# Kernel tuning notes

Hardware: AMD Instinct MI355X
Metric: run time of the kernel (lower is better)

## Reference

```python
import jax, jax.numpy as jnp
import numpy as np

L, B, S, H = 24, 32, 512, 1024   # layers, batch, pad_size, bert hidden
D_IN, D1, D2 = L * H, 900, 40     # 24576 -> 900 -> 40 -> 1


def setup_inputs() -> dict:
    key = jax.random.key(0)
    ks = jax.random.split(key, 8)
    hidden_states = jax.random.normal(ks[0], (L, B, S, H), dtype=jnp.float32)
    # monotonically increasing subword start indices; 0 == "no word starts here"
    bert_token_starts = jnp.sort(
        jax.random.randint(ks[1], (B, S), 0, S, dtype=jnp.int64), axis=-1)
    W1 = jax.random.normal(ks[2], (D_IN, D1), dtype=jnp.float32) * 0.02
    b1 = jnp.zeros((D1,), dtype=jnp.float32)
    W2 = jax.random.normal(ks[3], (D1, D2), dtype=jnp.float32) * 0.02
    b2 = jnp.zeros((D2,), dtype=jnp.float32)
    W3 = jax.random.normal(ks[4], (D2, 1), dtype=jnp.float32) * 0.02
    b3 = jnp.zeros((1,), dtype=jnp.float32)
    return {
        "hidden_states": hidden_states,
        "W1": W1, "b1": b1, "W2": W2, "b2": b2, "W3": W3, "b3": b3,
        "bert_token_starts": bert_token_starts,
    }


def reference(hidden_states, W1, b1, W2, b2, W3, b3, bert_token_starts):
    # torch.cat over 24 layers along dim=2  ->  [B, S, 24*H] (layer-major feature order)
    x = jnp.moveaxis(hidden_states, 0, 2).reshape(
        hidden_states.shape[1], hidden_states.shape[2], -1)  # [B, S, 24576]
    h = jax.nn.relu(x @ W1 + b1)                # [B, S, 900]
    h = jax.nn.relu(h @ W2 + b2)                # [B, S, 40]
    pred_logits = jax.nn.sigmoid(h @ W3 + b3)[..., 0]  # squeeze(2) -> [B, S]
    # ragged gather: pred_labels[b][w] = pred_logits[b][starts[b][w]] where start != 0
    # (starts are always < pad_size here; the st/end while-loop in the original is dead code)
    valid = bert_token_starts != 0
    idx = jnp.clip(bert_token_starts, 0, pred_logits.shape[1] - 1)
    gathered = jnp.take_along_axis(pred_logits, idx, axis=1)
    pred_labels = jnp.where(valid, gathered, jnp.zeros((), dtype=pred_logits.dtype))
    return pred_labels
```

## Files before the change

### kernel.cpp

```cpp
#include <hip/hip_runtime.h>

typedef __attribute__((ext_vector_type(8))) short bf16x8;
typedef __attribute__((ext_vector_type(4))) float f32x4;

#define L_DIM 24
#define B_DIM 32
#define S_DIM 512
#define H_DIM 1024
#define M_DIM 16384
#define K_DIM 24576
#define N_REAL 900
#define NP 1024

__device__ __forceinline__ short f2bf(float f) {
  unsigned u = __builtin_bit_cast(unsigned, f);
  u += 0x7FFFu + ((u >> 16) & 1u);
  return (short)(u >> 16);
}

__global__ __launch_bounds__(512)
void compact1_kernel(const int* __restrict__ starts, int* __restrict__ upos,
                     int* __restrict__ counts) {
  __shared__ int sc[512];
  const int b = blockIdx.x, t = threadIdx.x;
  const int v = starts[b * 512 + t];
  const int prev = (t > 0) ? starts[b * 512 + t - 1] : -1;
  const int flag = (v != 0 && v != prev) ? 1 : 0;
  sc[t] = flag;
  __syncthreads();
#pragma unroll
  for (int off = 1; off < 512; off <<= 1) {
    const int x = (t >= off) ? sc[t - off] : 0;
    __syncthreads();
    sc[t] += x;
    __syncthreads();
  }
  upos[b * 512 + t] = flag ? (sc[t] - 1) : -1;
  if (t == 511) counts[b] = sc[511];
}

__global__ __launch_bounds__(256)
void compact2_kernel(const int* __restrict__ counts, int* __restrict__ offs,
                     int* __restrict__ meta, int* __restrict__ idx) {
  __shared__ int s0, s1;
  if (threadIdx.x == 0) {
    int acc = 0;
    for (int b = 0; b < 32; ++b) { offs[b] = acc; acc += counts[b]; }
    meta[0] = acc;
    meta[1] = (acc + 255) & ~255;
    s0 = acc; s1 = (acc + 255) & ~255;
  }
  __syncthreads();
  for (int j = s0 + threadIdx.x; j < s1; j += 256) idx[j] = 0;
}

__global__ __launch_bounds__(512)
void compact3_kernel(const int* __restrict__ starts, const int* __restrict__ upos,
                     const int* __restrict__ offs, int* __restrict__ idx) {
  const int b = blockIdx.x, t = threadIdx.x;
  const int p = upos[b * 512 + t];
  if (p >= 0) idx[offs[b] + p] = b * 512 + starts[b * 512 + t];
}

__global__ __launch_bounds__(256)
void conv_a_kernel(const float* __restrict__ hs, const int* __restrict__ idx,
                   const int* __restrict__ meta, unsigned short* __restrict__ a) {
  const int mcp = meta[1];
  for (int j = blockIdx.x; j < mcp; j += gridDim.x) {
    const int m = idx[j];
    const int b = m >> 9, s = m & 511;
    const int j7 = j & 7;
    unsigned short* dstRow = a + (size_t)j * K_DIM;
#pragma unroll
    for (int i = 0; i < 12; ++i) {
      const int g = threadIdx.x + i * 256;
      const int l = g >> 7;
      const int h = (g & 127) * 8;
      const float* src = hs + (((size_t)l * B_DIM + b) * S_DIM + s) * H_DIM + h;
      float4 f0 = *(const float4*)src;
      float4 f1 = *(const float4*)(src + 4);
      bf16x8 p;
      p[0] = f2bf(f0.x); p[1] = f2bf(f0.y); p[2] = f2bf(f0.z); p[3] = f2bf(f0.w);
      p[4] = f2bf(f1.x); p[5] = f2bf(f1.y); p[6] = f2bf(f1.z); p[7] = f2bf(f1.w);
      const int slot = (g & 7) ^ j7;
      *(bf16x8*)(dstRow + (g & ~7) * 8 + slot * 8) = p;
    }
  }
}

__global__ __launch_bounds__(256)
void prep_w1t_kernel(const float* __restrict__ w1, unsigned short* __restrict__ w1t) {
  __shared__ unsigned short t[64][72];
  const int n0 = blockIdx.x * 64;
  const int k0 = blockIdx.y * 64;
  const int tid = threadIdx.x;
  {
    const int nl = tid & 63;
    const int n = n0 + nl;
#pragma unroll
    for (int p = 0; p < 16; ++p) {
      const int kl = p * 4 + (tid >> 6);
      float v = (n < N_REAL) ? w1[(size_t)(k0 + kl) * N_REAL + n] : 0.f;
      t[nl][kl] = (unsigned short)f2bf(v);
    }
  }
  __syncthreads();
  {
    const int kl = tid & 63;
#pragma unroll
    for (int p = 0; p < 16; ++p) {
      const int nl2 = p * 4 + (tid >> 6);
      const int n = n0 + nl2;
      const int slot = ((kl >> 3) ^ (n & 7)) & 7;
      w1t[(size_t)n * K_DIM + k0 + slot * 8 + (kl & 7)] = t[nl2][kl];
    }
  }
}

__global__ __launch_bounds__(256)
void prep_small_kernel(const float* __restrict__ w2, const float* __restrict__ b1,
                       float* __restrict__ w2t, float* __restrict__ b1p) {
  const int i = blockIdx.x * 256 + threadIdx.x;
  if (i < 40 * NP) {
    const int j = i >> 10, k = i & (NP - 1);
    w2t[i] = (k < N_REAL) ? w2[(size_t)k * 40 + j] : 0.f;
  }
  const int t2 = i - 40 * NP;
  if (t2 >= 0 && t2 < NP)
    b1p[t2] = (t2 < N_REAL) ? b1[t2] : 0.f;
}

#define SBAR() do { __builtin_amdgcn_sched_barrier(0); __builtin_amdgcn_s_barrier(); __builtin_amdgcn_sched_barrier(0); } while (0)
#define WAIT_LGKM0() do { asm volatile("s_waitcnt lgkmcnt(0)" ::: "memory"); __builtin_amdgcn_sched_barrier(0); } while (0)
#define VMWAIT(N) do { asm volatile("s_waitcnt vmcnt(" #N ")" ::: "memory"); __builtin_amdgcn_sched_barrier(0); } while (0)

#define STAGE(DSTREG, GBASE, ROWBASE, HALF, TK) do {                                   \
  _Pragma("unroll")                                                                    \
  for (int _i = 0; _i < 2; ++_i) {                                                     \
    const int _ch = wid * 2 + _i;                                                      \
    const int _row = (HALF) * 128 + _ch * 8 + (lane >> 3);                             \
    __builtin_amdgcn_global_load_lds(                                                  \
      (const __attribute__((address_space(1))) void*)((GBASE) +                        \
          (size_t)((ROWBASE) + _row) * K_DIM + (TK) * 64 + (lane & 7) * 8),            \
      (__attribute__((address_space(3))) void*)((DSTREG) + (HALF) * 16384 + _ch * 1024), \
      16, 0, 0);                                                                       \
  }                                                                                    \
} while (0)

#define LDA4(AV, MIBASE, ABUF) do {                                                    \
  _Pragma("unroll")                                                                    \
  for (int _mi = 0; _mi < 4; ++_mi) {                                                  \
    _Pragma("unroll")                                                                  \
    for (int _kk = 0; _kk < 2; ++_kk) {                                                \
      const int _r = ((MIBASE) >> 2) * 128 + wr * 64 + _mi * 16 + r15;                 \
      AV[_mi][_kk] = *(const bf16x8*)((ABUF) + _r * 128 + (((_kk)*4 + hi4) ^ (_r & 7)) * 16); \
    }                                                                                  \
  }                                                                                    \
} while (0)

#define LDB2(BV, NIBASE, BBUF) do {                                                    \
  _Pragma("unroll")                                                                    \
  for (int _ni = 0; _ni < 2; ++_ni) {                                                  \
    _Pragma("unroll")                                                                  \
    for (int _kk = 0; _kk < 2; ++_kk) {                                                \
      const int _r = ((NIBASE) >> 1) * 128 + wc * 32 + _ni * 16 + r15;                 \
      BV[_ni][_kk] = *(const bf16x8*)((BBUF) + _r * 128 + (((_kk)*4 + hi4) ^ (_r & 7)) * 16); \
    }                                                                                  \
  }                                                                                    \
} while (0)

#define MFMA_Q(AV, BV, MIBASE, NIBASE) do {                                            \
  _Pragma("unroll")                                                                    \
  for (int _mi = 0; _mi < 4; ++_mi)                                                    \
    _Pragma("unroll")                                                                  \
    for (int _ni = 0; _ni < 2; ++_ni)                                                  \
      _Pragma("unroll")                                                                \
      for (int _kk = 0; _kk < 2; ++_kk)                                                \
        acc[(MIBASE) + _mi][(NIBASE) + _ni] = __builtin_amdgcn_mfma_f32_16x16x32_bf16( \
            AV[_mi][_kk], BV[_ni][_kk], acc[(MIBASE) + _mi][(NIBASE) + _ni], 0, 0, 0); \
} while (0)

#define TILE_BODY(T, AB, BB, ABN, BBN, S1, S2, S3, S4, W1STMT, W4STMT) do {            \
                                                                \
  LDA4(av, 0, (AB));                                                                   \
  LDB2(bv0, 0, (BB));                                                                  \
  if (S1) STAGE((ABN), a, m0, 1, (T) + 1);                                             \
  SBAR();                                                                              \
  WAIT_LGKM0();                                                                        \
  __builtin_amdgcn_s_setprio(1);                                                       \
  MFMA_Q(av, bv0, 0, 0);                                                               \
  __builtin_amdgcn_s_setprio(0);                                                       \
  W1STMT;                                                                              \
  SBAR();                                                                              \
                                                                \
  LDB2(bv1, 2, (BB));                                                                  \
  if (S2) STAGE((BBN), w1t, n0, 1, (T) + 1);                                           \
  SBAR();                                                                              \
  WAIT_LGKM0();                                                                        \
  __builtin_amdgcn_s_setprio(1);                                                       \
  MFMA_Q(av, bv1, 0, 2);                                                               \
  __builtin_amdgcn_s_setprio(0);                                                       \
  SBAR();                                                                              \
                                                                \
  LDA4(av, 4, (AB));                                                                   \
  if (S3) STAGE((BB), w1t, n0, 0, (T) + 2);                                            \
  SBAR();                                                                              \
  WAIT_LGKM0();                                                                        \
  __builtin_amdgcn_s_setprio(1);                                                       \
  MFMA_Q(av, bv1, 4, 2);                                                               \
  __builtin_amdgcn_s_setprio(0);                                                       \
  SBAR();                                                                              \
                                                                \
  if (S4) STAGE((AB), a, m0, 0, (T) + 2);                                              \
  SBAR();                                                                              \
  WAIT_LGKM0();                                                                        \
  __builtin_amdgcn_s_setprio(1);                                                       \
  MFMA_Q(av, bv0, 4, 0);                                                               \
  __builtin_amdgcn_s_setprio(0);                                                       \
  W4STMT;                                                                              \
  SBAR();                                                                              \
} while (0)

__global__ __launch_bounds__(512, 2)
void gemm1_8ph_kernel(const unsigned short* __restrict__ a,
                      const unsigned short* __restrict__ w1t,
                      const float* __restrict__ b1p,
                      const int* __restrict__ meta,
                      float* __restrict__ h1) {
  const int mcp = meta[1];

  const int hw = blockIdx.x;
  const int c = hw & 7;
  const int r = hw >> 3;
  const int mb = (r >> 2) * 8 + c;
  const int nb = r & 3;
  const int m0 = mb * 256;
  if (m0 >= mcp) return;
  const int n0 = nb * 256;

  extern __shared__ char L[];
  char* const Ab0 = L;
  char* const Bb0 = L + 32768;
  char* const Ab1 = L + 65536;
  char* const Bb1 = L + 65536 + 32768;

  const int tid = threadIdx.x;
  const int lane = tid & 63;
  const int wid = tid >> 6;
  const int wr = wid >> 2;
  const int wc = wid & 3;
  const int r15 = lane & 15;
  const int hi4 = lane >> 4;

  f32x4 acc[8][4] = {};
  bf16x8 av[4][2], bv0[2][2], bv1[2][2];

  STAGE(Bb0, w1t, n0, 0, 0);
  STAGE(Ab0, a, m0, 0, 0);
  STAGE(Ab0, a, m0, 1, 0);
  STAGE(Bb0, w1t, n0, 1, 0);
  STAGE(Bb1, w1t, n0, 0, 1);
  STAGE(Ab1, a, m0, 0, 1);
  VMWAIT(8);
  SBAR();

  for (int kt = 0; kt < 191; ++kt) {
    const int t = 2 * kt;
    TILE_BODY(t,     Ab0, Bb0, Ab1, Bb1, 1, 1, 1, 1, VMWAIT(6), VMWAIT(8));
    TILE_BODY(t + 1, Ab1, Bb1, Ab0, Bb0, 1, 1, 1, 1, VMWAIT(6), VMWAIT(8));
  }
  TILE_BODY(382, Ab0, Bb0, Ab1, Bb1, 1, 1, 0, 0, VMWAIT(6), VMWAIT(0));
  TILE_BODY(383, Ab1, Bb1, Ab0, Bb0, 0, 0, 0, 0, (void)0, (void)0);

#pragma unroll
  for (int mi = 0; mi < 8; ++mi) {
#pragma unroll
    for (int ni = 0; ni < 4; ++ni) {
      const int n = n0 + (ni >> 1) * 128 + wc * 32 + (ni & 1) * 16 + r15;
      const float bias = b1p[n];
#pragma unroll
      for (int rr = 0; rr < 4; ++rr) {
        const int m = m0 + (mi >> 2) * 128 + wr * 64 + (mi & 3) * 16 + hi4 * 4 + rr;
        const float v = acc[mi][ni][rr] + bias;
        h1[(size_t)m * NP + n] = v > 0.f ? v : 0.f;
      }
    }
  }
}

__global__ __launch_bounds__(256)
void layer23_kernel(const float* __restrict__ h1, const float* __restrict__ w2t,
                    const float* __restrict__ b2, const float* __restrict__ w3,
                    const float* __restrict__ b3, const int* __restrict__ idx,
                    const int* __restrict__ meta, float* __restrict__ logits) {
  const int j = (blockIdx.x * 256 + threadIdx.x) >> 6;
  if (j >= meta[0]) return;
  const int lane = threadIdx.x & 63;
  const float* hrow = h1 + (size_t)j * NP;
  float acc = 0.f;
  if (lane < 40) {
    const float* wrow = w2t + lane * NP;
    for (int k = 0; k < NP; k += 8) {
      float4 h0 = *(const float4*)(hrow + k);
      float4 h4 = *(const float4*)(hrow + k + 4);
      float4 w0 = *(const float4*)(wrow + k);
      float4 w4 = *(const float4*)(wrow + k + 4);
      acc += h0.x * w0.x + h0.y * w0.y + h0.z * w0.z + h0.w * w0.w;
      acc += h4.x * w4.x + h4.y * w4.y + h4.z * w4.z + h4.w * w4.w;
    }
    acc += b2[lane];
    acc = acc > 0.f ? acc : 0.f;
    acc *= w3[lane];
  }
#pragma unroll
  for (int off = 32; off > 0; off >>= 1)
    acc += __shfl_down(acc, off);
  if (lane == 0)
    logits[idx[j]] = 1.f / (1.f + expf(-(acc + b3[0])));
}

__global__ __launch_bounds__(256)
void gather_kernel(const int* __restrict__ starts, const float* __restrict__ logits,
                   float* __restrict__ out) {
  const int i = blockIdx.x * 256 + threadIdx.x;
  if (i >= M_DIM) return;
  const int st = starts[i];
  int idx = st;
  if (idx < 0) idx = 0;
  if (idx > S_DIM - 1) idx = S_DIM - 1;
  out[i] = (st != 0) ? logits[((i >> 9) << 9) + idx] : 0.f;
}

extern "C" void kernel_launch(void* const* d_in, const int* in_sizes, int n_in,
                              void* d_out, int out_size, void* d_ws, size_t ws_size,
                              hipStream_t stream) {
  const float* hs = (const float*)d_in[0];
  const float* W1 = (const float*)d_in[1];
  const float* b1 = (const float*)d_in[2];
  const float* W2 = (const float*)d_in[3];
  const float* b2 = (const float*)d_in[4];
  const float* W3 = (const float*)d_in[5];
  const float* b3 = (const float*)d_in[6];
  const int* starts = (const int*)d_in[7];
  float* out = (float*)d_out;
  char* ws = (char*)d_ws;

  const size_t A_BYTES   = (size_t)M_DIM * K_DIM * 2;
  const size_t W1T_BYTES = (size_t)NP * K_DIM * 2;
  const size_t H1_BYTES  = (size_t)M_DIM * NP * 4;
  const size_t W2T_BYTES = 40 * NP * 4;
  const size_t B1P_BYTES = NP * 4;
  const size_t LG_BYTES  = M_DIM * 4;

  unsigned short* a    = (unsigned short*)ws;
  unsigned short* w1t  = (unsigned short*)(ws + A_BYTES);
  char* h1c            = ws + A_BYTES + W1T_BYTES;
  float* h1            = (float*)h1c;
  float* w2t           = (float*)(ws + A_BYTES + W1T_BYTES + H1_BYTES);
  float* b1p           = (float*)(ws + A_BYTES + W1T_BYTES + H1_BYTES + W2T_BYTES);
  float* logits        = (float*)(ws + A_BYTES + W1T_BYTES + H1_BYTES + W2T_BYTES + B1P_BYTES);
  int* idx             = (int*)(ws + A_BYTES + W1T_BYTES + H1_BYTES + W2T_BYTES + B1P_BYTES + LG_BYTES);
  int* meta            = (int*)(ws + A_BYTES + W1T_BYTES + H1_BYTES + W2T_BYTES + B1P_BYTES + LG_BYTES + 65536);
  int* upos            = (int*)h1c;
  int* counts          = (int*)(h1c + 65536);
  int* offs            = (int*)(h1c + 65536 + 128);

  hipFuncSetAttribute((const void*)gemm1_8ph_kernel,
                      hipFuncAttributeMaxDynamicSharedMemorySize, 131072);

  compact1_kernel<<<32, 512, 0, stream>>>(starts, upos, counts);
  compact2_kernel<<<1, 256, 0, stream>>>(counts, offs, meta, idx);
  compact3_kernel<<<32, 512, 0, stream>>>(starts, upos, offs, idx);
  conv_a_kernel<<<2048, 256, 0, stream>>>(hs, idx, meta, a);
  prep_w1t_kernel<<<dim3(16, 384), 256, 0, stream>>>(W1, w1t);
  prep_small_kernel<<<164, 256, 0, stream>>>(W2, b1, w2t, b1p);
  gemm1_8ph_kernel<<<256, 512, 131072, stream>>>(a, w1t, b1p, meta, h1);
  layer23_kernel<<<4096, 256, 0, stream>>>(h1, w2t, b2, W3, b3, idx, meta, logits);
  gather_kernel<<<64, 256, 0, stream>>>(starts, logits, out);
}
```

Before: 1.218 ms.

## Split GEMM1 K dimension three ways and reduce partials in layer23

GEMM1 now splits the K loop into three chunks of 128 tiles, launching three times as many workgroups, each writing an unbiased fp32 partial panel into its own buffer. The layer23 kernel sums the three partials, adds the bias and applies ReLU before the second layer. The aim is to fill more CUs when the compacted M is small, since 256 workgroups left many CUs idle. The cost is triple the h1 write and read traffic and a larger workspace.

```diff
diff --git a/kernel.cpp b/kernel.cpp
--- a/kernel.cpp
+++ b/kernel.cpp
@@ -224,19 +224,20 @@
 __global__ __launch_bounds__(512, 2)
 void gemm1_8ph_kernel(const unsigned short* __restrict__ a,
                       const unsigned short* __restrict__ w1t,
-                      const float* __restrict__ b1p,
                       const int* __restrict__ meta,
-                      float* __restrict__ h1) {
+                      float* __restrict__ h1p) {
   const int mcp = meta[1];
+  const int n_panels = mcp >> 8;
 
   const int hw = blockIdx.x;
-  const int c = hw & 7;
-  const int r = hw >> 3;
-  const int mb = (r >> 2) * 8 + c;
-  const int nb = r & 3;
+  const int mb = hw / 12;
+  if (mb >= n_panels) return;
+  const int rem = hw - mb * 12;
+  const int nb = rem & 3;
+  const int kh = rem >> 2;
   const int m0 = mb * 256;
-  if (m0 >= mcp) return;
   const int n0 = nb * 256;
+  const int t0 = kh * 128;
 
   extern __shared__ char L[];
   char* const Ab0 = L;
@@ -255,58 +256,64 @@
   f32x4 acc[8][4] = {};
   bf16x8 av[4][2], bv0[2][2], bv1[2][2];
 
-  STAGE(Bb0, w1t, n0, 0, 0);
-  STAGE(Ab0, a, m0, 0, 0);
-  STAGE(Ab0, a, m0, 1, 0);
-  STAGE(Bb0, w1t, n0, 1, 0);
-  STAGE(Bb1, w1t, n0, 0, 1);
-  STAGE(Ab1, a, m0, 0, 1);
+  STAGE(Bb0, w1t, n0, 0, t0);
+  STAGE(Ab0, a, m0, 0, t0);
+  STAGE(Ab0, a, m0, 1, t0);
+  STAGE(Bb0, w1t, n0, 1, t0);
+  STAGE(Bb1, w1t, n0, 0, t0 + 1);
+  STAGE(Ab1, a, m0, 0, t0 + 1);
   VMWAIT(8);
   SBAR();
 
-  for (int kt = 0; kt < 191; ++kt) {
-    const int t = 2 * kt;
+  for (int kt = 0; kt < 63; ++kt) {
+    const int t = t0 + 2 * kt;
     TILE_BODY(t,     Ab0, Bb0, Ab1, Bb1, 1, 1, 1, 1, VMWAIT(6), VMWAIT(8));
     TILE_BODY(t + 1, Ab1, Bb1, Ab0, Bb0, 1, 1, 1, 1, VMWAIT(6), VMWAIT(8));
   }
-  TILE_BODY(382, Ab0, Bb0, Ab1, Bb1, 1, 1, 0, 0, VMWAIT(6), VMWAIT(0));
-  TILE_BODY(383, Ab1, Bb1, Ab0, Bb0, 0, 0, 0, 0, (void)0, (void)0);
-
+  TILE_BODY(t0 + 126, Ab0, Bb0, Ab1, Bb1, 1, 1, 0, 0, VMWAIT(6), VMWAIT(0));
+  TILE_BODY(t0 + 127, Ab1, Bb1, Ab0, Bb0, 0, 0, 0, 0, (void)0, (void)0);
+
+  float* dst = h1p + (size_t)kh * ((size_t)M_DIM * NP);
 #pragma unroll
   for (int mi = 0; mi < 8; ++mi) {
 #pragma unroll
     for (int ni = 0; ni < 4; ++ni) {
       const int n = n0 + (ni >> 1) * 128 + wc * 32 + (ni & 1) * 16 + r15;
-      const float bias = b1p[n];
 #pragma unroll
       for (int rr = 0; rr < 4; ++rr) {
         const int m = m0 + (mi >> 2) * 128 + wr * 64 + (mi & 3) * 16 + hi4 * 4 + rr;
-        const float v = acc[mi][ni][rr] + bias;
-        h1[(size_t)m * NP + n] = v > 0.f ? v : 0.f;
+        dst[(size_t)m * NP + n] = acc[mi][ni][rr];
       }
     }
   }
 }
 
 __global__ __launch_bounds__(256)
-void layer23_kernel(const float* __restrict__ h1, const float* __restrict__ w2t,
-                    const float* __restrict__ b2, const float* __restrict__ w3,
-                    const float* __restrict__ b3, const int* __restrict__ idx,
-                    const int* __restrict__ meta, float* __restrict__ logits) {
+void layer23_kernel(const float* __restrict__ h1p, const float* __restrict__ w2t,
+                    const float* __restrict__ b1p, const float* __restrict__ b2,
+                    const float* __restrict__ w3, const float* __restrict__ b3,
+                    const int* __restrict__ idx, const int* __restrict__ meta,
+                    float* __restrict__ logits) {
   const int j = (blockIdx.x * 256 + threadIdx.x) >> 6;
   if (j >= meta[0]) return;
   const int lane = threadIdx.x & 63;
-  const float* hrow = h1 + (size_t)j * NP;
+  const float* p0 = h1p + (size_t)j * NP;
+  const float* p1 = p0 + (size_t)M_DIM * NP;
+  const float* p2 = p1 + (size_t)M_DIM * NP;
   float acc = 0.f;
   if (lane < 40) {
     const float* wrow = w2t + lane * NP;
-    for (int k = 0; k < NP; k += 8) {
-      float4 h0 = *(const float4*)(hrow + k);
-      float4 h4 = *(const float4*)(hrow + k + 4);
+    for (int k = 0; k < NP; k += 4) {
+      float4 a0 = *(const float4*)(p0 + k);
+      float4 a1 = *(const float4*)(p1 + k);
+      float4 a2 = *(const float4*)(p2 + k);
+      float4 bb = *(const float4*)(b1p + k);
       float4 w0 = *(const float4*)(wrow + k);
-      float4 w4 = *(const float4*)(wrow + k + 4);
-      acc += h0.x * w0.x + h0.y * w0.y + h0.z * w0.z + h0.w * w0.w;
-      acc += h4.x * w4.x + h4.y * w4.y + h4.z * w4.z + h4.w * w4.w;
+      float x0 = a0.x + a1.x + a2.x + bb.x; x0 = x0 > 0.f ? x0 : 0.f;
+      float x1 = a0.y + a1.y + a2.y + bb.y; x1 = x1 > 0.f ? x1 : 0.f;
+      float x2 = a0.z + a1.z + a2.z + bb.z; x2 = x2 > 0.f ? x2 : 0.f;
+      float x3 = a0.w + a1.w + a2.w + bb.w; x3 = x3 > 0.f ? x3 : 0.f;
+      acc += x0 * w0.x + x1 * w0.y + x2 * w0.z + x3 * w0.w;
     }
     acc += b2[lane];
     acc = acc > 0.f ? acc : 0.f;
@@ -347,7 +354,7 @@
 
   const size_t A_BYTES   = (size_t)M_DIM * K_DIM * 2;
   const size_t W1T_BYTES = (size_t)NP * K_DIM * 2;
-  const size_t H1_BYTES  = (size_t)M_DIM * NP * 4;
+  const size_t H1P_BYTES = 3ull * M_DIM * NP * 4;
   const size_t W2T_BYTES = 40 * NP * 4;
   const size_t B1P_BYTES = NP * 4;
   const size_t LG_BYTES  = M_DIM * 4;
@@ -355,12 +362,12 @@
   unsigned short* a    = (unsigned short*)ws;
   unsigned short* w1t  = (unsigned short*)(ws + A_BYTES);
   char* h1c            = ws + A_BYTES + W1T_BYTES;
-  float* h1            = (float*)h1c;
-  float* w2t           = (float*)(ws + A_BYTES + W1T_BYTES + H1_BYTES);
-  float* b1p           = (float*)(ws + A_BYTES + W1T_BYTES + H1_BYTES + W2T_BYTES);
-  float* logits        = (float*)(ws + A_BYTES + W1T_BYTES + H1_BYTES + W2T_BYTES + B1P_BYTES);
-  int* idx             = (int*)(ws + A_BYTES + W1T_BYTES + H1_BYTES + W2T_BYTES + B1P_BYTES + LG_BYTES);
-  int* meta            = (int*)(ws + A_BYTES + W1T_BYTES + H1_BYTES + W2T_BYTES + B1P_BYTES + LG_BYTES + 65536);
+  float* h1p           = (float*)h1c;
+  float* w2t           = (float*)(ws + A_BYTES + W1T_BYTES + H1P_BYTES);
+  float* b1p           = (float*)(ws + A_BYTES + W1T_BYTES + H1P_BYTES + W2T_BYTES);
+  float* logits        = (float*)(ws + A_BYTES + W1T_BYTES + H1P_BYTES + W2T_BYTES + B1P_BYTES);
+  int* idx             = (int*)(ws + A_BYTES + W1T_BYTES + H1P_BYTES + W2T_BYTES + B1P_BYTES + LG_BYTES);
+  int* meta            = (int*)(ws + A_BYTES + W1T_BYTES + H1P_BYTES + W2T_BYTES + B1P_BYTES + LG_BYTES + 65536);
   int* upos            = (int*)h1c;
   int* counts          = (int*)(h1c + 65536);
   int* offs            = (int*)(h1c + 65536 + 128);
@@ -374,7 +381,7 @@
   conv_a_kernel<<<2048, 256, 0, stream>>>(hs, idx, meta, a);
   prep_w1t_kernel<<<dim3(16, 384), 256, 0, stream>>>(W1, w1t);
   prep_small_kernel<<<164, 256, 0, stream>>>(W2, b1, w2t, b1p);
-  gemm1_8ph_kernel<<<256, 512, 131072, stream>>>(a, w1t, b1p, meta, h1);
-  layer23_kernel<<<4096, 256, 0, stream>>>(h1, w2t, b2, W3, b3, idx, meta, logits);
+  gemm1_8ph_kernel<<<768, 512, 131072, stream>>>(a, w1t, meta, h1p);
+  layer23_kernel<<<4096, 256, 0, stream>>>(h1p, w2t, b1p, b2, W3, b3, idx, meta, logits);
   gather_kernel<<<64, 256, 0, stream>>>(starts, logits, out);
 }
```

Result: no change. 1.241 ms (+1.9%).

## Shrink GEMM1 M-tile to 192 rows to cut padding waste and balance CUs

Applied to the files above, without the earlier changes.

Changes the first-layer GEMM tile from 256x256 to 192x256. The compacted row count is now padded to a multiple of 192 instead of 256, and the grid grows to 352 blocks. The A staging, LDS layout, MFMA quadrant schedule and pipeline wait counts are reworked to match, and the workspace is enlarged to cover the extra padded rows. The aim is less wasted compute on padded rows and a better spread of blocks over the CUs. The cost is lower per-block arithmetic intensity, more B reloads and a retuned pipeline that may stall differently.

```diff
diff --git a/kernel.cpp b/kernel.cpp
--- a/kernel.cpp
+++ b/kernel.cpp
@@ -11,6 +11,7 @@
 #define K_DIM 24576
 #define N_REAL 900
 #define NP 1024
+#define BM 192
 
 __device__ __forceinline__ short f2bf(float f) {
   unsigned u = __builtin_bit_cast(unsigned, f);
@@ -46,9 +47,10 @@
   if (threadIdx.x == 0) {
     int acc = 0;
     for (int b = 0; b < 32; ++b) { offs[b] = acc; acc += counts[b]; }
+    const int pad = ((acc + BM - 1) / BM) * BM;
     meta[0] = acc;
-    meta[1] = (acc + 255) & ~255;
-    s0 = acc; s1 = (acc + 255) & ~255;
+    meta[1] = pad;
+    s0 = acc; s1 = pad;
   }
   __syncthreads();
   for (int j = s0 + threadIdx.x; j < s1; j += 256) idx[j] = 0;
@@ -134,25 +136,38 @@
 #define WAIT_LGKM0() do { asm volatile("s_waitcnt lgkmcnt(0)" ::: "memory"); __builtin_amdgcn_sched_barrier(0); } while (0)
 #define VMWAIT(N) do { asm volatile("s_waitcnt vmcnt(" #N ")" ::: "memory"); __builtin_amdgcn_sched_barrier(0); } while (0)
 
-#define STAGE(DSTREG, GBASE, ROWBASE, HALF, TK) do {                                   \
+#define STAGE_A(DSTREG, TK) do {                                                       \
+  _Pragma("unroll")                                                                    \
+  for (int _i = 0; _i < 3; ++_i) {                                                     \
+    const int _ch = wid * 3 + _i;                                                      \
+    const int _row = _ch * 8 + (lane >> 3);                                            \
+    __builtin_amdgcn_global_load_lds(                                                  \
+      (const __attribute__((address_space(1))) void*)(a +                              \
+          (size_t)(m0 + _row) * K_DIM + (TK) * 64 + (lane & 7) * 8),                   \
+      (__attribute__((address_space(3))) void*)((DSTREG) + _ch * 1024),                \
+      16, 0, 0);                                                                       \
+  }                                                                                    \
+} while (0)
+
+#define STAGE_B(DSTREG, HALF, TK) do {                                                 \
   _Pragma("unroll")                                                                    \
   for (int _i = 0; _i < 2; ++_i) {                                                     \
     const int _ch = wid * 2 + _i;                                                      \
     const int _row = (HALF) * 128 + _ch * 8 + (lane >> 3);                             \
     __builtin_amdgcn_global_load_lds(                                                  \
-      (const __attribute__((address_space(1))) void*)((GBASE) +                        \
-          (size_t)((ROWBASE) + _row) * K_DIM + (TK) * 64 + (lane & 7) * 8),            \
+      (const __attribute__((address_space(1))) void*)(w1t +                            \
+          (size_t)(n0 + _row) * K_DIM + (TK) * 64 + (lane & 7) * 8),                   \
       (__attribute__((address_space(3))) void*)((DSTREG) + (HALF) * 16384 + _ch * 1024), \
       16, 0, 0);                                                                       \
   }                                                                                    \
 } while (0)
 
-#define LDA4(AV, MIBASE, ABUF) do {                                                    \
-  _Pragma("unroll")                                                                    \
-  for (int _mi = 0; _mi < 4; ++_mi) {                                                  \
+#define LDA3(AV, MIBASE, ABUF) do {                                                    \
+  _Pragma("unroll")                                                                    \
+  for (int _mi = 0; _mi < 3; ++_mi) {                                                  \
     _Pragma("unroll")                                                                  \
     for (int _kk = 0; _kk < 2; ++_kk) {                                                \
-      const int _r = ((MIBASE) >> 2) * 128 + wr * 64 + _mi * 16 + r15;                 \
+      const int _r = ((MIBASE) / 3) * 96 + wr * 48 + _mi * 16 + r15;                   \
       AV[_mi][_kk] = *(const bf16x8*)((ABUF) + _r * 128 + (((_kk)*4 + hi4) ^ (_r & 7)) * 16); \
     }                                                                                  \
   }                                                                                    \
@@ -171,7 +186,7 @@
 
 #define MFMA_Q(AV, BV, MIBASE, NIBASE) do {                                            \
   _Pragma("unroll")                                                                    \
-  for (int _mi = 0; _mi < 4; ++_mi)                                                    \
+  for (int _mi = 0; _mi < 3; ++_mi)                                                    \
     _Pragma("unroll")                                                                  \
     for (int _ni = 0; _ni < 2; ++_ni)                                                  \
       _Pragma("unroll")                                                                \
@@ -180,69 +195,61 @@
             AV[_mi][_kk], BV[_ni][_kk], acc[(MIBASE) + _mi][(NIBASE) + _ni], 0, 0, 0); \
 } while (0)
 
-#define TILE_BODY(T, AB, BB, ABN, BBN, S1, S2, S3, S4, W1STMT, W4STMT) do {            \
-                                                                \
-  LDA4(av, 0, (AB));                                                                   \
+#define TILE_BODY(T, AB, BB, ABN, BBN, S1, S2, S3, WAITSTMT) do {                      \
+                                                       \
+  LDA3(av, 0, (AB));                                                                   \
   LDB2(bv0, 0, (BB));                                                                  \
-  if (S1) STAGE((ABN), a, m0, 1, (T) + 1);                                             \
+  if (S1) STAGE_A((ABN), (T) + 1);                                                     \
   SBAR();                                                                              \
   WAIT_LGKM0();                                                                        \
   __builtin_amdgcn_s_setprio(1);                                                       \
   MFMA_Q(av, bv0, 0, 0);                                                               \
   __builtin_amdgcn_s_setprio(0);                                                       \
-  W1STMT;                                                                              \
-  SBAR();                                                                              \
-                                                                \
+  SBAR();                                                                              \
+                                                       \
   LDB2(bv1, 2, (BB));                                                                  \
-  if (S2) STAGE((BBN), w1t, n0, 1, (T) + 1);                                           \
+  if (S2) STAGE_B((BBN), 1, (T) + 1);                                                  \
   SBAR();                                                                              \
   WAIT_LGKM0();                                                                        \
   __builtin_amdgcn_s_setprio(1);                                                       \
   MFMA_Q(av, bv1, 0, 2);                                                               \
   __builtin_amdgcn_s_setprio(0);                                                       \
   SBAR();                                                                              \
-                                                                \
-  LDA4(av, 4, (AB));                                                                   \
-  if (S3) STAGE((BB), w1t, n0, 0, (T) + 2);                                            \
+                                                 \
+  LDA3(av, 3, (AB));                                                                   \
+  if (S3) STAGE_B((BB), 0, (T) + 2);                                                   \
   SBAR();                                                                              \
   WAIT_LGKM0();                                                                        \
   __builtin_amdgcn_s_setprio(1);                                                       \
-  MFMA_Q(av, bv1, 4, 2);                                                               \
+  MFMA_Q(av, bv1, 3, 2);                                                               \
+  MFMA_Q(av, bv0, 3, 0);                                                               \
   __builtin_amdgcn_s_setprio(0);                                                       \
-  SBAR();                                                                              \
-                                                                \
-  if (S4) STAGE((AB), a, m0, 0, (T) + 2);                                              \
-  SBAR();                                                                              \
-  WAIT_LGKM0();                                                                        \
-  __builtin_amdgcn_s_setprio(1);                                                       \
-  MFMA_Q(av, bv0, 4, 0);                                                               \
-  __builtin_amdgcn_s_setprio(0);                                                       \
-  W4STMT;                                                                              \
+  WAITSTMT;                                                                            \
   SBAR();                                                                              \
 } while (0)
 
 __global__ __launch_bounds__(512, 2)
-void gemm1_8ph_kernel(const unsigned short* __restrict__ a,
+void gemm1_192_kernel(const unsigned short* __restrict__ a,
                       const unsigned short* __restrict__ w1t,
                       const float* __restrict__ b1p,
                       const int* __restrict__ meta,
                       float* __restrict__ h1) {
-  const int mcp = meta[1];
+  const int n_panels = meta[1] / BM;
 
   const int hw = blockIdx.x;
   const int c = hw & 7;
   const int r = hw >> 3;
   const int mb = (r >> 2) * 8 + c;
+  if (mb >= n_panels) return;
   const int nb = r & 3;
-  const int m0 = mb * 256;
-  if (m0 >= mcp) return;
+  const int m0 = mb * BM;
   const int n0 = nb * 256;
 
   extern __shared__ char L[];
   char* const Ab0 = L;
-  char* const Bb0 = L + 32768;
-  char* const Ab1 = L + 65536;
-  char* const Bb1 = L + 65536 + 32768;
+  char* const Ab1 = L + 24576;
+  char* const Bb0 = L + 49152;
+  char* const Bb1 = L + 49152 + 32768;
 
   const int tid = threadIdx.x;
   const int lane = tid & 63;
@@ -252,35 +259,33 @@
   const int r15 = lane & 15;
   const int hi4 = lane >> 4;
 
-  f32x4 acc[8][4] = {};
-  bf16x8 av[4][2], bv0[2][2], bv1[2][2];
-
-  STAGE(Bb0, w1t, n0, 0, 0);
-  STAGE(Ab0, a, m0, 0, 0);
-  STAGE(Ab0, a, m0, 1, 0);
-  STAGE(Bb0, w1t, n0, 1, 0);
-  STAGE(Bb1, w1t, n0, 0, 1);
-  STAGE(Ab1, a, m0, 0, 1);
-  VMWAIT(8);
+  f32x4 acc[6][4] = {};
+  bf16x8 av[3][2], bv0[2][2], bv1[2][2];
+
+  STAGE_B(Bb0, 0, 0);
+  STAGE_A(Ab0, 0);
+  STAGE_B(Bb0, 1, 0);
+  STAGE_B(Bb1, 0, 1);
+  VMWAIT(2);
   SBAR();
 
   for (int kt = 0; kt < 191; ++kt) {
     const int t = 2 * kt;
-    TILE_BODY(t,     Ab0, Bb0, Ab1, Bb1, 1, 1, 1, 1, VMWAIT(6), VMWAIT(8));
-    TILE_BODY(t + 1, Ab1, Bb1, Ab0, Bb0, 1, 1, 1, 1, VMWAIT(6), VMWAIT(8));
-  }
-  TILE_BODY(382, Ab0, Bb0, Ab1, Bb1, 1, 1, 0, 0, VMWAIT(6), VMWAIT(0));
-  TILE_BODY(383, Ab1, Bb1, Ab0, Bb0, 0, 0, 0, 0, (void)0, (void)0);
-
-#pragma unroll
-  for (int mi = 0; mi < 8; ++mi) {
+    TILE_BODY(t,     Ab0, Bb0, Ab1, Bb1, 1, 1, 1, VMWAIT(2));
+    TILE_BODY(t + 1, Ab1, Bb1, Ab0, Bb0, 1, 1, 1, VMWAIT(2));
+  }
+  TILE_BODY(382, Ab0, Bb0, Ab1, Bb1, 1, 1, 0, VMWAIT(0));
+  TILE_BODY(383, Ab1, Bb1, Ab0, Bb0, 0, 0, 0, (void)0);
+
+#pragma unroll
+  for (int mi = 0; mi < 6; ++mi) {
 #pragma unroll
     for (int ni = 0; ni < 4; ++ni) {
       const int n = n0 + (ni >> 1) * 128 + wc * 32 + (ni & 1) * 16 + r15;
       const float bias = b1p[n];
 #pragma unroll
       for (int rr = 0; rr < 4; ++rr) {
-        const int m = m0 + (mi >> 2) * 128 + wr * 64 + (mi & 3) * 16 + hi4 * 4 + rr;
+        const int m = m0 + (mi / 3) * 96 + wr * 48 + (mi % 3) * 16 + hi4 * 4 + rr;
         const float v = acc[mi][ni][rr] + bias;
         h1[(size_t)m * NP + n] = v > 0.f ? v : 0.f;
       }
@@ -345,9 +350,9 @@
   float* out = (float*)d_out;
   char* ws = (char*)d_ws;
 
-  const size_t A_BYTES   = (size_t)M_DIM * K_DIM * 2;
+  const size_t A_BYTES   = (size_t)(M_DIM + 256) * K_DIM * 2;
   const size_t W1T_BYTES = (size_t)NP * K_DIM * 2;
-  const size_t H1_BYTES  = (size_t)M_DIM * NP * 4;
+  const size_t H1_BYTES  = (size_t)(M_DIM + 256) * NP * 4;
   const size_t W2T_BYTES = 40 * NP * 4;
   const size_t B1P_BYTES = NP * 4;
   const size_t LG_BYTES  = M_DIM * 4;
@@ -360,13 +365,13 @@
   float* b1p           = (float*)(ws + A_BYTES + W1T_BYTES + H1_BYTES + W2T_BYTES);
   float* logits        = (float*)(ws + A_BYTES + W1T_BYTES + H1_BYTES + W2T_BYTES + B1P_BYTES);
   int* idx             = (int*)(ws + A_BYTES + W1T_BYTES + H1_BYTES + W2T_BYTES + B1P_BYTES + LG_BYTES);
-  int* meta            = (int*)(ws + A_BYTES + W1T_BYTES + H1_BYTES + W2T_BYTES + B1P_BYTES + LG_BYTES + 65536);
+  int* meta            = (int*)(ws + A_BYTES + W1T_BYTES + H1_BYTES + W2T_BYTES + B1P_BYTES + LG_BYTES + 66560);
   int* upos            = (int*)h1c;
   int* counts          = (int*)(h1c + 65536);
   int* offs            = (int*)(h1c + 65536 + 128);
 
-  hipFuncSetAttribute((const void*)gemm1_8ph_kernel,
-                      hipFuncAttributeMaxDynamicSharedMemorySize, 131072);
+  hipFuncSetAttribute((const void*)gemm1_192_kernel,
+                      hipFuncAttributeMaxDynamicSharedMemorySize, 114688);
 
   compact1_kernel<<<32, 512, 0, stream>>>(starts, upos, counts);
   compact2_kernel<<<1, 256, 0, stream>>>(counts, offs, meta, idx);
@@ -374,7 +379,7 @@
   conv_a_kernel<<<2048, 256, 0, stream>>>(hs, idx, meta, a);
   prep_w1t_kernel<<<dim3(16, 384), 256, 0, stream>>>(W1, w1t);
   prep_small_kernel<<<164, 256, 0, stream>>>(W2, b1, w2t, b1p);
-  gemm1_8ph_kernel<<<256, 512, 131072, stream>>>(a, w1t, b1p, meta, h1);
+  gemm1_192_kernel<<<352, 512, 114688, stream>>>(a, w1t, b1p, meta, h1);
   layer23_kernel<<<4096, 256, 0, stream>>>(h1, w2t, b2, W3, b3, idx, meta, logits);
   gather_kernel<<<64, 256, 0, stream>>>(starts, logits, out);
 }
```

After: 1.111 ms. 1.1x faster.
